# Performance work log

Hardware: AMD Instinct MI355X
Metric: run time of the kernel (lower is better)

## Reference

```python
import jax, jax.numpy as jnp
import numpy as np

B, N, D = 64, 2048, 64
KC = 512
BETA = 0.5


def setup_inputs() -> dict:
    key = jax.random.key(0)
    k1, k2, k3 = jax.random.split(key, 3)
    F_active = jax.random.normal(k1, (B, N, D), dtype=jnp.float32)
    centers = jax.random.normal(k2, (KC, D), dtype=jnp.float32)
    psi = 0.1 * jax.random.normal(k3, (KC,), dtype=jnp.float32)
    beta = jnp.float32(BETA)
    return {"F_active": F_active, "centers": centers, "psi": psi, "beta": beta}


def reference(F_active, centers, psi, beta):
    # Squared Euclidean distance via GEMM expansion (avoids the (B,N,Kc,d) diff tensor):
    # ||f - c||^2 = ||f||^2 + ||c||^2 - 2 f.c
    f2 = jnp.sum(F_active * F_active, axis=-1, keepdims=True)          # (B, N, 1)
    c2 = jnp.sum(centers * centers, axis=-1)                           # (Kc,)
    fc = jnp.einsum('bnd,kd->bnk', F_active, centers)                  # (B, N, Kc)
    dist2 = jnp.maximum(f2 + c2[None, None, :] - 2.0 * fc, 0.0)       # (B, N, Kc)
    sim = jnp.exp(-beta * dist2)                                       # (B, N, Kc)
    w = jax.nn.softmax(psi, axis=0)                                    # (Kc,)
    score_per_slot = jnp.einsum('bnk,k->bn', sim, w)                   # (B, N)
    return jnp.mean(score_per_slot, axis=1)                            # (B,)
```

## Files before the change

kernel.cpp:

```cpp
#include <hip/hip_runtime.h>

typedef _Float16 f16x8 __attribute__((ext_vector_type(8)));
typedef float f32x4 __attribute__((ext_vector_type(4)));

static constexpr float kLog2e = 1.44269504088896340736f;

#define WS_EW 65536

__device__ __forceinline__ float fast_exp2(float x) {
#if __has_builtin(__builtin_amdgcn_exp2f)
  return __builtin_amdgcn_exp2f(x);
#else
  return exp2f(x);
#endif
}

__global__ __launch_bounds__(512) void prep_kernel(
    const float* __restrict__ centers, const float* __restrict__ psi,
    const float* __restrict__ beta, _Float16* __restrict__ cfrag,
    float2* __restrict__ ew, float* __restrict__ out) {
  __shared__ float red[8];
  const int n = threadIdx.x;
  const int lane = n & 63;
  const int wid = n >> 6;
  const float b = beta[0];
  const float kco = -b * kLog2e;

  float4 row[16];
  const float4* crow = (const float4*)(centers + n * 64);
  float c2 = 0.f;
#pragma unroll
  for (int i = 0; i < 16; ++i) {
    row[i] = crow[i];
    c2 = fmaf(row[i].x, row[i].x, c2); c2 = fmaf(row[i].y, row[i].y, c2);
    c2 = fmaf(row[i].z, row[i].z, c2); c2 = fmaf(row[i].w, row[i].w, c2);
  }

  const float p = psi[n];
  float m = p;
#pragma unroll
  for (int d = 1; d < 64; d <<= 1) m = fmaxf(m, __shfl_xor(m, d, 64));
  if (lane == 0) red[wid] = m;
  __syncthreads();
  float mx = red[0];
#pragma unroll
  for (int i = 1; i < 8; ++i) mx = fmaxf(mx, red[i]);
  __syncthreads();
  const float ex = fast_exp2((p - mx) * kLog2e);
  float ssum = ex;
#pragma unroll
  for (int d = 1; d < 64; d <<= 1) ssum += __shfl_xor(ssum, d, 64);
  if (lane == 0) red[wid] = ssum;
  __syncthreads();
  float tot = 0.f;
#pragma unroll
  for (int i = 0; i < 8; ++i) tot += red[i];

  ew[n] = make_float2(kco * c2, ex / tot);

  const int t = n >> 4;
  const int l15 = n & 15;
#pragma unroll
  for (int kk = 0; kk < 2; ++kk) {
#pragma unroll
    for (int quad = 0; quad < 4; ++quad) {
      const int idx = (t * 2 + kk) * 64 + quad * 16 + l15;
      const float4 v0 = row[kk * 8 + quad * 2];
      const float4 v1 = row[kk * 8 + quad * 2 + 1];
      f16x8 h;
      h[0] = (_Float16)v0.x; h[1] = (_Float16)v0.y;
      h[2] = (_Float16)v0.z; h[3] = (_Float16)v0.w;
      h[4] = (_Float16)v1.x; h[5] = (_Float16)v1.y;
      h[6] = (_Float16)v1.z; h[7] = (_Float16)v1.w;
      *(f16x8*)(cfrag + (size_t)idx * 8) = h;
    }
  }

  if (n < 64) out[n] = 0.f;
}

__global__ __launch_bounds__(256, 2) void score_kernel(
    const float* __restrict__ F, const _Float16* __restrict__ cfrag,
    const float2* __restrict__ ew, const float* __restrict__ beta,
    float* __restrict__ out) {
  __shared__ float f2s[256];
  __shared__ float wsum[4];
  const int tid = threadIdx.x;
  const int lane = tid & 63;
  const int wv = tid >> 6;
  const int quad = lane >> 4;
  const int l15 = lane & 15;
  const int R0 = blockIdx.x * 256;

  const float b = beta[0];
  const float cC = 2.f * b * kLog2e;
  const float kco = -b * kLog2e;

  f16x8 a[4][2];
#pragma unroll
  for (int rt = 0; rt < 4; ++rt) {
    const int row = R0 + wv * 64 + rt * 16 + l15;
    const float* fr = F + row * 64 + quad * 8;
    float ssq = 0.f;
#pragma unroll
    for (int kk = 0; kk < 2; ++kk) {
      const float4 v0 = *(const float4*)(fr + kk * 32);
      const float4 v1 = *(const float4*)(fr + kk * 32 + 4);
      ssq = fmaf(v0.x, v0.x, ssq); ssq = fmaf(v0.y, v0.y, ssq);
      ssq = fmaf(v0.z, v0.z, ssq); ssq = fmaf(v0.w, v0.w, ssq);
      ssq = fmaf(v1.x, v1.x, ssq); ssq = fmaf(v1.y, v1.y, ssq);
      ssq = fmaf(v1.z, v1.z, ssq); ssq = fmaf(v1.w, v1.w, ssq);
      a[rt][kk][0] = (_Float16)(cC * v0.x); a[rt][kk][1] = (_Float16)(cC * v0.y);
      a[rt][kk][2] = (_Float16)(cC * v0.z); a[rt][kk][3] = (_Float16)(cC * v0.w);
      a[rt][kk][4] = (_Float16)(cC * v1.x); a[rt][kk][5] = (_Float16)(cC * v1.y);
      a[rt][kk][6] = (_Float16)(cC * v1.z); a[rt][kk][7] = (_Float16)(cC * v1.w);
    }
    ssq += __shfl_xor(ssq, 16, 64);
    ssq += __shfl_xor(ssq, 32, 64);
    if (quad == 0) f2s[wv * 64 + rt * 16 + l15] = ssq;
  }
  __syncthreads();

  float p0[4][4];
#pragma unroll
  for (int rt = 0; rt < 4; ++rt)
#pragma unroll
    for (int r = 0; r < 4; ++r)
      p0[rt][r] = kco * f2s[wv * 64 + rt * 16 + quad * 4 + r];

  float s = 0.f;
#pragma unroll 2
  for (int t = 0; t < 32; ++t) {
    const f16x8 b0 = *(const f16x8*)(cfrag + (size_t)((t * 2 + 0) * 64 + lane) * 8);
    const f16x8 b1 = *(const f16x8*)(cfrag + (size_t)((t * 2 + 1) * 64 + lane) * 8);
    const float2 ewv = ew[t * 16 + l15];
    float esum = 0.f;
#pragma unroll
    for (int rt = 0; rt < 4; ++rt) {
      f32x4 acc = {p0[rt][0] + ewv.x, p0[rt][1] + ewv.x,
                   p0[rt][2] + ewv.x, p0[rt][3] + ewv.x};
      acc = __builtin_amdgcn_mfma_f32_16x16x32_f16(a[rt][0], b0, acc, 0, 0, 0);
      acc = __builtin_amdgcn_mfma_f32_16x16x32_f16(a[rt][1], b1, acc, 0, 0, 0);
#pragma unroll
      for (int r = 0; r < 4; ++r)
        esum += fast_exp2(fminf(acc[r], 0.f));
    }
    s = fmaf(ewv.y, esum, s);
  }

#pragma unroll
  for (int d = 1; d < 64; d <<= 1) s += __shfl_xor(s, d, 64);
  if (lane == 0) wsum[wv] = s;
  __syncthreads();
  if (tid == 0) {
    const float tot = wsum[0] + wsum[1] + wsum[2] + wsum[3];
    atomicAdd(out + (blockIdx.x >> 3), tot * (1.0f / 2048.0f));
  }
}

extern "C" void kernel_launch(void* const* d_in, const int* in_sizes, int n_in,
                              void* d_out, int out_size, void* d_ws, size_t ws_size,
                              hipStream_t stream) {
  const float* F = (const float*)d_in[0];
  const float* centers = (const float*)d_in[1];
  const float* psi = (const float*)d_in[2];
  const float* beta = (const float*)d_in[3];
  float* out = (float*)d_out;
  char* ws = (char*)d_ws;
  _Float16* cfrag = (_Float16*)ws;
  float2* ew = (float2*)(ws + WS_EW);

  prep_kernel<<<1, 512, 0, stream>>>(centers, psi, beta, cfrag, ew, out);
  score_kernel<<<512, 256, 0, stream>>>(F, cfrag, ew, beta, out);
}
```

Measured before the change: 100.3 us.

## Split center range across two wave groups and parallelize prep over blocks

The score kernel now launches 512 threads per block. Two groups of four waves share the same 256 rows, and each group processes half of the 512 centers, so the blocks hold more waves in flight. The prep kernel is split into 8 single-wave blocks. Each block recomputes the psi softmax normalizer with vectorized loads and shuffles only, with no LDS barriers. The cost is that both wave groups load F and convert it to fp16 redundantly, and each wave now holds its own A fragments, which raises register and occupancy pressure.

```diff
diff --git a/kernel.cpp b/kernel.cpp
--- a/kernel.cpp
+++ b/kernel.cpp
@@ -15,19 +15,17 @@
 #endif
 }
 
-__global__ __launch_bounds__(512) void prep_kernel(
+__global__ __launch_bounds__(64) void prep_kernel(
     const float* __restrict__ centers, const float* __restrict__ psi,
     const float* __restrict__ beta, _Float16* __restrict__ cfrag,
     float2* __restrict__ ew, float* __restrict__ out) {
-  __shared__ float red[8];
-  const int n = threadIdx.x;
-  const int lane = n & 63;
-  const int wid = n >> 6;
+  const int tid = threadIdx.x;
+  const int c = blockIdx.x * 64 + tid;
   const float b = beta[0];
   const float kco = -b * kLog2e;
 
   float4 row[16];
-  const float4* crow = (const float4*)(centers + n * 64);
+  const float4* crow = (const float4*)(centers + c * 64);
   float c2 = 0.f;
 #pragma unroll
   for (int i = 0; i < 16; ++i) {
@@ -36,30 +34,23 @@
     c2 = fmaf(row[i].z, row[i].z, c2); c2 = fmaf(row[i].w, row[i].w, c2);
   }
 
-  const float p = psi[n];
-  float m = p;
+  const float4 pv0 = *(const float4*)(psi + tid * 8);
+  const float4 pv1 = *(const float4*)(psi + tid * 8 + 4);
+  float m = fmaxf(fmaxf(fmaxf(pv0.x, pv0.y), fmaxf(pv0.z, pv0.w)),
+                  fmaxf(fmaxf(pv1.x, pv1.y), fmaxf(pv1.z, pv1.w)));
 #pragma unroll
   for (int d = 1; d < 64; d <<= 1) m = fmaxf(m, __shfl_xor(m, d, 64));
-  if (lane == 0) red[wid] = m;
-  __syncthreads();
-  float mx = red[0];
+  float ls = fast_exp2((pv0.x - m) * kLog2e) + fast_exp2((pv0.y - m) * kLog2e) +
+             fast_exp2((pv0.z - m) * kLog2e) + fast_exp2((pv0.w - m) * kLog2e) +
+             fast_exp2((pv1.x - m) * kLog2e) + fast_exp2((pv1.y - m) * kLog2e) +
+             fast_exp2((pv1.z - m) * kLog2e) + fast_exp2((pv1.w - m) * kLog2e);
 #pragma unroll
-  for (int i = 1; i < 8; ++i) mx = fmaxf(mx, red[i]);
-  __syncthreads();
-  const float ex = fast_exp2((p - mx) * kLog2e);
-  float ssum = ex;
-#pragma unroll
-  for (int d = 1; d < 64; d <<= 1) ssum += __shfl_xor(ssum, d, 64);
-  if (lane == 0) red[wid] = ssum;
-  __syncthreads();
-  float tot = 0.f;
-#pragma unroll
-  for (int i = 0; i < 8; ++i) tot += red[i];
+  for (int d = 1; d < 64; d <<= 1) ls += __shfl_xor(ls, d, 64);
+  const float ex = fast_exp2((psi[c] - m) * kLog2e);
+  ew[c] = make_float2(kco * c2, ex / ls);
 
-  ew[n] = make_float2(kco * c2, ex / tot);
-
-  const int t = n >> 4;
-  const int l15 = n & 15;
+  const int t = c >> 4;
+  const int l15 = c & 15;
 #pragma unroll
   for (int kk = 0; kk < 2; ++kk) {
 #pragma unroll
@@ -76,18 +67,20 @@
     }
   }
 
-  if (n < 64) out[n] = 0.f;
+  if (blockIdx.x == 0) out[tid] = 0.f;
 }
 
-__global__ __launch_bounds__(256, 2) void score_kernel(
+__global__ __launch_bounds__(512, 4) void score_kernel(
     const float* __restrict__ F, const _Float16* __restrict__ cfrag,
     const float2* __restrict__ ew, const float* __restrict__ beta,
     float* __restrict__ out) {
   __shared__ float f2s[256];
-  __shared__ float wsum[4];
+  __shared__ float wsum[8];
   const int tid = threadIdx.x;
   const int lane = tid & 63;
   const int wv = tid >> 6;
+  const int rg = wv >> 2;
+  const int wr = wv & 3;
   const int quad = lane >> 4;
   const int l15 = lane & 15;
   const int R0 = blockIdx.x * 256;
@@ -99,7 +92,7 @@
   f16x8 a[4][2];
 #pragma unroll
   for (int rt = 0; rt < 4; ++rt) {
-    const int row = R0 + wv * 64 + rt * 16 + l15;
+    const int row = R0 + wr * 64 + rt * 16 + l15;
     const float* fr = F + row * 64 + quad * 8;
     float ssq = 0.f;
 #pragma unroll
@@ -117,7 +110,7 @@
     }
     ssq += __shfl_xor(ssq, 16, 64);
     ssq += __shfl_xor(ssq, 32, 64);
-    if (quad == 0) f2s[wv * 64 + rt * 16 + l15] = ssq;
+    if (rg == 0 && quad == 0) f2s[wr * 64 + rt * 16 + l15] = ssq;
   }
   __syncthreads();
 
@@ -126,11 +119,13 @@
   for (int rt = 0; rt < 4; ++rt)
 #pragma unroll
     for (int r = 0; r < 4; ++r)
-      p0[rt][r] = kco * f2s[wv * 64 + rt * 16 + quad * 4 + r];
+      p0[rt][r] = kco * f2s[wr * 64 + rt * 16 + quad * 4 + r];
 
   float s = 0.f;
+  const int tbase = rg * 16;
 #pragma unroll 2
-  for (int t = 0; t < 32; ++t) {
+  for (int ti = 0; ti < 16; ++ti) {
+    const int t = tbase + ti;
     const f16x8 b0 = *(const f16x8*)(cfrag + (size_t)((t * 2 + 0) * 64 + lane) * 8);
     const f16x8 b1 = *(const f16x8*)(cfrag + (size_t)((t * 2 + 1) * 64 + lane) * 8);
     const float2 ewv = ew[t * 16 + l15];
@@ -153,7 +148,9 @@
   if (lane == 0) wsum[wv] = s;
   __syncthreads();
   if (tid == 0) {
-    const float tot = wsum[0] + wsum[1] + wsum[2] + wsum[3];
+    float tot = 0.f;
+#pragma unroll
+    for (int i = 0; i < 8; ++i) tot += wsum[i];
     atomicAdd(out + (blockIdx.x >> 3), tot * (1.0f / 2048.0f));
   }
 }
@@ -170,6 +167,6 @@
   _Float16* cfrag = (_Float16*)ws;
   float2* ew = (float2*)(ws + WS_EW);
 
-  prep_kernel<<<1, 512, 0, stream>>>(centers, psi, beta, cfrag, ew, out);
-  score_kernel<<<512, 256, 0, stream>>>(F, cfrag, ew, beta, out);
+  prep_kernel<<<8, 64, 0, stream>>>(centers, psi, beta, cfrag, ew, out);
+  score_kernel<<<512, 512, 0, stream>>>(F, cfrag, ew, beta, out);
 }
```

Result: faster. 97.75 us (-2.6%).
